# Optimization experiments

Hardware: AMD Instinct MI355X
Metric: run time of the kernel (lower is better)

The kernel has to match this reference:

```python
import jax, jax.numpy as jnp
import numpy as np

BS, T, Q, HID, PROJ = 16, 16, 100, 256, 256


def setup_inputs() -> dict:
    key = jax.random.key(0)
    k1, k2, k3, k4, k5 = jax.random.split(key, 5)
    frame_embeds = jax.random.normal(k1, (BS, T, Q, HID), jnp.float32)
    other_frame_embeds = jax.random.normal(k2, (BS, T, Q, HID), jnp.float32)
    W = jax.random.normal(k3, (HID, PROJ), jnp.float32) / np.sqrt(HID).astype(np.float32)
    b = jax.random.normal(k4, (PROJ,), jnp.float32) * 0.01
    n = BS * Q
    mid = jax.random.randint(k5, (n, 1), 1, T - 1, dtype=jnp.int32)
    bridge = jnp.concatenate(
        [jnp.zeros((n, 1), jnp.int32), mid, jnp.full((n, 1), T - 1, jnp.int32)], axis=1
    )  # (n,3): head=0, random pivot in [1,T-2], tail=T-1
    return {"frame_embeds": frame_embeds, "other_frame_embeds": other_frame_embeds,
            "W": W, "b": b, "bridge": bridge}


def _prep(fe, W, b):
    # Linear proj, (bs,t,q,c)->(bs*q, t, c), L2-normalize per embedding.
    bs, t, q, _ = fe.shape
    x = fe @ W + b
    x = x.transpose(0, 2, 1, 3).reshape(bs * q, t, -1)
    return x / jnp.linalg.norm(x, axis=-1, keepdims=True)


def _forward(frame_embeds, other_frame_embeds, W, b, bridge, delta=0.3):
    cur = _prep(frame_embeds, W, b)      # (n,t,c)
    other = _prep(other_frame_embeds, W, b)
    bh = bridge[:, 0].astype(jnp.float32)
    bp_f = bridge[:, 1].astype(jnp.float32)
    bt = bridge[:, 2].astype(jnp.float32)
    alpha = (bp_f - bh) / (bt - bh)      # (n,)
    sigma = alpha * (bt - bp_f)          # (n,)
    g = jnp.take_along_axis(cur, bridge[:, :, None], axis=1)  # (n,3,c) head/pivot/tail
    # positive brownian-bridge distance
    x = g[:, 1] - (1.0 - alpha)[:, None] * g[:, 0] - alpha[:, None] * g[:, 2]
    numer = jnp.exp(-jnp.sum(x * x, axis=-1) / (2.0 * sigma ** 2))  # (n,)
    # negatives: pivot frame taken from every sequence in [cur; other].
    # ||m_ij - a_i||^2 = ||m_ij||^2 - 2 m_ij.a_i + ||a_i||^2 with m_ij = neg_all[j, bp_i],
    # avoiding the (n,N,3,c) repeat tensor of the original.
    neg_all = jnp.concatenate([cur, other], axis=0)            # (N,t,c)
    a = (1.0 - alpha)[:, None] * g[:, 0] + alpha[:, None] * g[:, 2]  # (n,c)
    cross = jnp.einsum('ic,jtc->ijt', a, neg_all)              # (n,N,t)
    bp = bridge[:, 1]
    cross_g = jnp.take_along_axis(cross, bp[:, None, None], axis=2)[..., 0]  # (n,N)
    nn2_g = jnp.sum(neg_all * neg_all, axis=-1).T[bp]          # (n,N)
    x2 = nn2_g - 2.0 * cross_g + jnp.sum(a * a, axis=-1)[:, None]
    dist = -x2 / (2.0 * sigma ** 2)[:, None]                   # (n,N)
    n = dist.shape[0]
    idx = jnp.arange(n)
    self_dist = dist[idx, idx]
    dist = dist.at[idx, idx].set(-10000.0)
    topv, _ = jax.lax.top_k(dist, 5)
    deno = jnp.exp(jnp.concatenate([self_dist[:, None], topv], axis=-1))  # (n,6)
    brownian_loss = (numer / deno.sum(axis=-1)).mean()
    score = jnp.einsum('nc,nc->n', cur[:, 0], cur[:, -1])
    head_tail_match = jax.nn.softplus(delta - score).mean()
    return brownian_loss, head_tail_match


def reference(frame_embeds, other_frame_embeds, W, b, bridge):
    return _forward(frame_embeds, other_frame_embeds, W, b, bridge)
```

## Files before the change

kernel.cpp:

```cpp
#include <hip/hip_runtime.h>
#include <hip/hip_bf16.h>

#define NROW 1600
#define NEG  3200
#define ROWS_FLAT 25600
#define NSPLIT 25

using bf16x8 = __attribute__((ext_vector_type(8))) short;
using f32x4  = __attribute__((ext_vector_type(4))) float;

__device__ __forceinline__ float bf2f(unsigned v) { return __uint_as_float(v << 16); }
__device__ __forceinline__ ushort f2bf(float f) {
  __hip_bfloat16 h = __float2bfloat16(f);
  return *(ushort*)&h;
}
__device__ __forceinline__ float load1(const ushort* p, size_t idx, int f32) {
  return f32 ? ((const float*)p)[idx] : bf2f(p[idx]);
}
__device__ __forceinline__ int sniff_f32(const ushort* p, int lane) {
  unsigned e = ((unsigned)p[2*lane] >> 7) & 0xffu;
  unsigned long long b = __ballot(e >= 100u && e <= 140u);
  return (__popcll(b) >= 40) ? 0 : 1;
}
__device__ __forceinline__ bf16x8 cvt8b(const float* a, const float* b) {
  float4 fa = *(const float4*)a;
  float4 fb = *(const float4*)b;
  bf16x8 r;
  r[0]=(short)f2bf(fa.x); r[1]=(short)f2bf(fa.y); r[2]=(short)f2bf(fa.z); r[3]=(short)f2bf(fa.w);
  r[4]=(short)f2bf(fb.x); r[5]=(short)f2bf(fb.y); r[6]=(short)f2bf(fb.z); r[7]=(short)f2bf(fb.w);
  return r;
}

__global__ __launch_bounds__(256) void k_prep(const ushort* __restrict__ W,
    ushort* __restrict__ Wtf, int* __restrict__ zbase) {
  if (blockIdx.x == 0 && threadIdx.x < 21) zbase[threadIdx.x] = 0;
  int fW = sniff_f32(W, threadIdx.x & 63);
  int n = blockIdx.x, k = threadIdx.x;
  int n16 = n >> 4, m = n & 15, kb = k >> 5, q = (k >> 3) & 3, e = k & 7;
  Wtf[(size_t)(n16*8 + kb)*512 + q*128 + m*8 + e] =
      f2bf(load1(W, (size_t)k * 256 + n, fW));
}

__global__ __launch_bounds__(256) void k_proj(const ushort* __restrict__ fe0,
    const ushort* __restrict__ fe1, const ushort* __restrict__ Wtf,
    const ushort* __restrict__ bias, const int* __restrict__ bridge,
    ushort* __restrict__ Pb, ushort* __restrict__ Ab, float* __restrict__ prm,
    float* __restrict__ numer, int* __restrict__ cnt, int* __restrict__ lst,
    float* __restrict__ wsum) {
  __shared__ union {
    float  xf[32*256];
    ushort x[32*256];
    ushort c[4][32*72];
  } sh;
  __shared__ float s_ss[4][32];
  __shared__ float s_bb[4][2][3];
  __shared__ int   s_brg[2][3];
  const int tid = threadIdx.x;
  const int w = tid >> 6, lane = tid & 63, q = lane >> 4, m = lane & 15;
  const int I0 = blockIdx.x * 2;
  const int hasB = (I0 < NROW);
  const int s1 = (I0 >= NROW);
  const ushort* srcp = s1 ? fe1 : fe0;
  const int fSrc = sniff_f32(srcp, lane);
  const int fB   = sniff_f32(bias, lane);
  if (hasB && tid < 6) s_brg[tid/3][tid%3] = bridge[(I0 + tid/3)*3 + tid%3];
  {
    int ii = I0 - s1*NROW + (w >> 1);
    int b = ii / 100, qq = ii - b*100;
    const size_t ub = (size_t)(b*1600 + qq) * 256;
    if (fSrc) {
      const float* fp = (const float*)srcp;
      #pragma unroll
      for (int i2 = 0; i2 < 8; i2++) {
        int r = w*8 + i2;
        int t = r & 15;
        int g = lane ^ (i2 & 7);
        const float* gp = fp + ub + (size_t)t*25600 + g*4;
        __builtin_amdgcn_global_load_lds(
          (const __attribute__((address_space(1))) unsigned int*)gp,
          (__attribute__((address_space(3))) unsigned int*)&sh.xf[r*256], 16, 0, 0);
      }
    } else {
      #pragma unroll
      for (int i2 = 0; i2 < 4; i2++) {
        int c = w*4 + i2;
        int r  = 2*c + (lane >> 5);
        int t  = r & 15;
        int kc = (lane & 31) ^ (r & 7);
        const ushort* gp = srcp + ub + (size_t)t*25600 + kc*8;
        __builtin_amdgcn_global_load_lds(
          (const __attribute__((address_space(1))) unsigned int*)gp,
          (__attribute__((address_space(3))) unsigned int*)&sh.x[c*512], 16, 0, 0);
      }
    }
  }
  __syncthreads();
  f32x4 acc[2][4];
  #pragma unroll
  for (int nt = 0; nt < 4; nt++) {
    float bb = load1(bias, w*64 + nt*16 + m, fB);
    f32x4 v = {bb, bb, bb, bb};
    #pragma unroll
    for (int mt = 0; mt < 2; mt++) acc[mt][nt] = v;
  }
  const int sw = (m & 7) << 3;
  const ushort* wfb = Wtf + (size_t)(w*4)*4096 + lane*8;
  bf16x8 a_cur[2], b_cur[4];
  if (fSrc) {
    int g0 = (q*2) ^ (m&7), g1 = (q*2 + 1) ^ (m&7);
    #pragma unroll
    for (int mt = 0; mt < 2; mt++)
      a_cur[mt] = cvt8b(&sh.xf[(mt*16+m)*256 + g0*4], &sh.xf[(mt*16+m)*256 + g1*4]);
  } else {
    #pragma unroll
    for (int mt = 0; mt < 2; mt++)
      a_cur[mt] = *(const bf16x8*)&sh.x[(mt*16 + m)*256 + ((q*8) ^ sw)];
  }
  #pragma unroll
  for (int nt = 0; nt < 4; nt++)
    b_cur[nt] = *(const bf16x8*)(wfb + (size_t)nt*4096);
  #pragma unroll
  for (int k = 0; k < 8; k++) {
    bf16x8 a_nxt[2], b_nxt[4];
    if (k < 7) {
      #pragma unroll
      for (int nt = 0; nt < 4; nt++)
        b_nxt[nt] = *(const bf16x8*)(wfb + (size_t)nt*4096 + (k+1)*512);
      if (fSrc) {
        int g0 = ((k+1)*8 + q*2) ^ (m&7), g1 = ((k+1)*8 + q*2 + 1) ^ (m&7);
        #pragma unroll
        for (int mt = 0; mt < 2; mt++)
          a_nxt[mt] = cvt8b(&sh.xf[(mt*16+m)*256 + g0*4], &sh.xf[(mt*16+m)*256 + g1*4]);
      } else {
        int pk = ((k+1)*32 + q*8) ^ sw;
        #pragma unroll
        for (int mt = 0; mt < 2; mt++)
          a_nxt[mt] = *(const bf16x8*)&sh.x[(mt*16 + m)*256 + pk];
      }
    }
    #pragma unroll
    for (int nt = 0; nt < 4; nt++)
      #pragma unroll
      for (int mt = 0; mt < 2; mt++)
        acc[mt][nt] = __builtin_amdgcn_mfma_f32_16x16x32_bf16(a_cur[mt], b_cur[nt], acc[mt][nt], 0, 0, 0);
    if (k < 7) {
      a_cur[0] = a_nxt[0]; a_cur[1] = a_nxt[1];
      #pragma unroll
      for (int x = 0; x < 4; x++) b_cur[x] = b_nxt[x];
    }
  }
  float ssp[2][4];
  #pragma unroll
  for (int mt = 0; mt < 2; mt++)
    #pragma unroll
    for (int reg = 0; reg < 4; reg++) {
      float s = 0.f;
      #pragma unroll
      for (int nt = 0; nt < 4; nt++) { float v = acc[mt][nt][reg]; s += v*v; }
      ssp[mt][reg] = s;
    }
  #pragma unroll
  for (int mk = 1; mk < 16; mk <<= 1)
    #pragma unroll
    for (int mt = 0; mt < 2; mt++)
      #pragma unroll
      for (int reg = 0; reg < 4; reg++) ssp[mt][reg] += __shfl_xor(ssp[mt][reg], mk, 64);
  if (m == 0)
    #pragma unroll
    for (int mt = 0; mt < 2; mt++)
      #pragma unroll
      for (int reg = 0; reg < 4; reg++) s_ss[w][mt*16 + 4*q + reg] = ssp[mt][reg];
  __syncthreads();
  float inv[2][4];
  #pragma unroll
  for (int mt = 0; mt < 2; mt++)
    #pragma unroll
    for (int reg = 0; reg < 4; reg++) {
      int row = mt*16 + 4*q + reg;
      float s = s_ss[0][row] + s_ss[1][row] + s_ss[2][row] + s_ss[3][row];
      inv[mt][reg] = 1.0f / sqrtf(s);
    }
  #pragma unroll
  for (int mt = 0; mt < 2; mt++)
    #pragma unroll
    for (int reg = 0; reg < 4; reg++) {
      int rl = mt*16 + 4*q + reg;
      #pragma unroll
      for (int nt = 0; nt < 4; nt++)
        sh.c[w][rl*72 + nt*16 + m] = f2bf(acc[mt][nt][reg] * inv[mt][reg]);
    }
  __syncthreads();
  #pragma unroll
  for (int p = 0; p < 4; p++) {
    int row = p*8 + (tid >> 5);
    int ig  = row >> 4, t = row & 15;
    int I   = I0 + ig;
    int ch  = tid & 31;
    uint4 v = *(uint4*)&sh.c[ch >> 3][row*72 + (ch & 7)*8];
    *(uint4*)(Pb + ((size_t)t * NEG + I) * 256 + ch*8) = v;
  }
  if (hasB) {
    #pragma unroll
    for (int ih = 0; ih < 2; ih++) {
      int bh = s_brg[ih][0], bp = s_brg[ih][1], bt = s_brg[ih][2];
      float alpha = ((float)bp - (float)bh) / ((float)bt - (float)bh);
      int rb = ih*16;
      float g0 = bf2f(sh.c[w][(rb + bh)*72 + lane]);
      float g1 = bf2f(sh.c[w][(rb + bp)*72 + lane]);
      float g2 = bf2f(sh.c[w][(rb + bt)*72 + lane]);
      float hd = bf2f(sh.c[w][(rb +  0)*72 + lane]);
      float tl = bf2f(sh.c[w][(rb + 15)*72 + lane]);
      float a = (1.0f - alpha) * g0 + alpha * g2;
      float x = g1 - a;
      int I = I0 + ih;
      Ab[(size_t)I*256 + w*64 + lane] = f2bf(a);
      float xx = x*x, aa = a*a, sc = hd*tl;
      #pragma unroll
      for (int mk = 1; mk < 64; mk <<= 1) {
        xx += __shfl_xor(xx, mk, 64);
        aa += __shfl_xor(aa, mk, 64);
        sc += __shfl_xor(sc, mk, 64);
      }
      if (lane == 0) { s_bb[w][ih][0] = xx; s_bb[w][ih][1] = aa; s_bb[w][ih][2] = sc; }
    }
    __syncthreads();
    if (tid < 2) {
      int I = I0 + tid;
      float XX = s_bb[0][tid][0] + s_bb[1][tid][0] + s_bb[2][tid][0] + s_bb[3][tid][0];
      float AA = s_bb[0][tid][1] + s_bb[1][tid][1] + s_bb[2][tid][1] + s_bb[3][tid][1];
      float SC = s_bb[0][tid][2] + s_bb[1][tid][2] + s_bb[2][tid][2] + s_bb[3][tid][2];
      int bh = s_brg[tid][0], bp = s_brg[tid][1], bt = s_brg[tid][2];
      float alpha = ((float)bp - (float)bh) / ((float)bt - (float)bh);
      float sigma = alpha * ((float)bt - (float)bp);
      float inv2s2 = 1.0f / (2.0f * sigma * sigma);
      prm[I*2+0] = inv2s2;
      prm[I*2+1] = AA;
      numer[I] = expf(-XX * inv2s2);
      float sp = log1pf(expf(0.3f - SC));
      atomicAdd(wsum + 1, sp * (1.0f / 1600.0f));
      int pos = atomicAdd(cnt + bp, 1);
      lst[bp * 1600 + pos] = I;
    }
  }
}

__device__ __forceinline__ void sort5(float* c) {
  #define CE(i,j) { float hi = fmaxf(c[i], c[j]), lo = fminf(c[i], c[j]); c[i]=hi; c[j]=lo; }
  CE(0,1) CE(3,4) CE(2,4) CE(2,3) CE(1,4) CE(0,3) CE(0,2) CE(1,3) CE(1,2)
  #undef CE
}
__device__ __forceinline__ void ins5(float* t, float v) {
  float hi, lo;
  hi = fmaxf(t[0], v); lo = fminf(t[0], v); t[0] = hi; v = lo;
  hi = fmaxf(t[1], v); lo = fminf(t[1], v); t[1] = hi; v = lo;
  hi = fmaxf(t[2], v); lo = fminf(t[2], v); t[2] = hi; v = lo;
  hi = fmaxf(t[3], v); lo = fminf(t[3], v); t[3] = hi; v = lo;
  t[4] = fmaxf(t[4], v);
}

__global__ __launch_bounds__(256) void k_cross(const ushort* __restrict__ Pb,
    const ushort* __restrict__ Ab, const float* __restrict__ prm,
    const int* __restrict__ cnt, const int* __restrict__ lst,
    float* __restrict__ part) {
  int t = blockIdx.z;
  int n_t = min(cnt[t], 1600);
  int i0 = blockIdx.y * 64;
  if (i0 >= n_t) return;
  int j0 = blockIdx.x * 128;
  __shared__ int s_gis[64];
  __shared__ float s_red[4][64][6];
  int tid = threadIdx.x;
  if (tid < 64) {
    int gi = lst[t*1600 + min(i0 + tid, n_t - 1)];
    s_gis[tid] = min(max(gi, 0), NROW - 1);
  }
  __syncthreads();
  const int w = tid >> 6, lane = tid & 63, q = lane >> 4, m = lane & 15;
  const ushort* jp0 = Pb + ((size_t)t * NEG + (j0 + w*32 + m)) * 256 + q*8;
  const ushort* jp1 = jp0 + (size_t)16*256;
  int gi[4];
  const ushort* ip[4];
  #pragma unroll
  for (int it = 0; it < 4; it++) {
    gi[it] = s_gis[it*16 + m];
    ip[it] = Ab + (size_t)gi[it] * 256 + q*8;
  }
  f32x4 acc[2][4];
  #pragma unroll
  for (int jt = 0; jt < 2; jt++)
    #pragma unroll
    for (int it = 0; it < 4; it++) { f32x4 z = {0.f,0.f,0.f,0.f}; acc[jt][it] = z; }
  bf16x8 jc0 = *(const bf16x8*)(jp0);
  bf16x8 jc1 = *(const bf16x8*)(jp1);
  bf16x8 ic[4];
  #pragma unroll
  for (int it = 0; it < 4; it++) ic[it] = *(const bf16x8*)(ip[it]);
  #pragma unroll
  for (int k = 0; k < 8; k++) {
    bf16x8 jn0, jn1, in[4];
    if (k < 7) {
      int o = (k + 1) * 32;
      jn0 = *(const bf16x8*)(jp0 + o);
      jn1 = *(const bf16x8*)(jp1 + o);
      #pragma unroll
      for (int it = 0; it < 4; it++) in[it] = *(const bf16x8*)(ip[it] + o);
    }
    __builtin_amdgcn_s_setprio(1);
    #pragma unroll
    for (int it = 0; it < 4; it++) {
      acc[0][it] = __builtin_amdgcn_mfma_f32_16x16x32_bf16(jc0, ic[it], acc[0][it], 0, 0, 0);
      acc[1][it] = __builtin_amdgcn_mfma_f32_16x16x32_bf16(jc1, ic[it], acc[1][it], 0, 0, 0);
    }
    __builtin_amdgcn_s_setprio(0);
    if (k < 7) { jc0 = jn0; jc1 = jn1;
      #pragma unroll
      for (int it = 0; it < 4; it++) ic[it] = in[it];
    }
  }
  float top[4][5], selfv[4];
  float pi[4], pa[4];
  #pragma unroll
  for (int it = 0; it < 4; it++) {
    pi[it] = prm[gi[it]*2]; pa[it] = prm[gi[it]*2+1];
    selfv[it] = -1e30f;
    #pragma unroll
    for (int k = 0; k < 5; k++) top[it][k] = -1e30f;
  }
  #pragma unroll
  for (int jt = 0; jt < 2; jt++)
    #pragma unroll
    for (int reg = 0; reg < 4; reg++) {
      int j = j0 + w*32 + jt*16 + 4*q + reg;
      #pragma unroll
      for (int it = 0; it < 4; it++) {
        float d = -(1.0f - 2.0f*acc[jt][it][reg] + pa[it]) * pi[it];
        if (j == gi[it]) selfv[it] = d; else ins5(top[it], d);
      }
    }
  #pragma unroll
  for (int mk = 16; mk <= 32; mk <<= 1) {
    #pragma unroll
    for (int it = 0; it < 4; it++) {
      float o[5], c[5];
      #pragma unroll
      for (int k = 0; k < 5; k++) o[k] = __shfl_xor(top[it][k], mk, 64);
      #pragma unroll
      for (int k = 0; k < 5; k++) c[k] = fmaxf(top[it][k], o[4 - k]);
      sort5(c);
      #pragma unroll
      for (int k = 0; k < 5; k++) top[it][k] = c[k];
      selfv[it] = fmaxf(selfv[it], __shfl_xor(selfv[it], mk, 64));
    }
  }
  if (q == 0) {
    #pragma unroll
    for (int it = 0; it < 4; it++) {
      #pragma unroll
      for (int k = 0; k < 5; k++) s_red[w][it*16 + m][k] = top[it][k];
      s_red[w][it*16 + m][5] = selfv[it];
    }
  }
  __syncthreads();
  if (tid < 64 && i0 + tid < n_t) {
    float T[5], S = s_red[0][tid][5];
    #pragma unroll
    for (int k = 0; k < 5; k++) T[k] = s_red[0][tid][k];
    #pragma unroll
    for (int w2 = 1; w2 < 4; w2++) {
      #pragma unroll
      for (int k = 0; k < 5; k++) ins5(T, s_red[w2][tid][k]);
      S = fmaxf(S, s_red[w2][tid][5]);
    }
    float* pp = part + ((size_t)s_gis[tid]*NSPLIT + blockIdx.x) * 6;
    #pragma unroll
    for (int k = 0; k < 5; k++) pp[k] = T[k];
    pp[5] = S;
  }
}

__global__ __launch_bounds__(64) void k_merge(const float* __restrict__ part,
    const float* __restrict__ numer, float* __restrict__ wsum, int* __restrict__ done,
    const ushort* __restrict__ fe0, void* __restrict__ out) {
  int i = blockIdx.x * 64 + threadIdx.x;
  const float* pp = part + (size_t)i * NSPLIT * 6;
  float T[5]; float S = pp[5];
  #pragma unroll
  for (int k = 0; k < 5; k++) T[k] = pp[k];
  #pragma unroll
  for (int s = 1; s < NSPLIT; s++) {
    const float* ps = pp + s*6;
    float v0 = ps[0], v1 = ps[1], v2 = ps[2], v3 = ps[3], v4 = ps[4], v5 = ps[5];
    ins5(T, v0); ins5(T, v1); ins5(T, v2); ins5(T, v3); ins5(T, v4);
    S = fmaxf(S, v5);
  }
  float deno = expf(S);
  #pragma unroll
  for (int k = 0; k < 5; k++) deno += expf(T[k]);
  float local = numer[i] / deno;
  #pragma unroll
  for (int mk = 1; mk < 64; mk <<= 1) local += __shfl_xor(local, mk, 64);
  __shared__ int s_last;
  if (threadIdx.x == 0) {
    atomicAdd(wsum + 0, local * (1.0f / 1600.0f));
    __threadfence();
    s_last = (atomicAdd(done, 1) == 24);
  }
  __syncthreads();
  if (s_last) {
    int f = sniff_f32(fe0, threadIdx.x);
    if (threadIdx.x == 0) {
      __threadfence();
      float brown = __hip_atomic_load(wsum + 0, __ATOMIC_RELAXED, __HIP_MEMORY_SCOPE_AGENT);
      float sp    = __hip_atomic_load(wsum + 1, __ATOMIC_RELAXED, __HIP_MEMORY_SCOPE_AGENT);
      if (f) {
        ((float*)out)[0] = brown;
        ((float*)out)[1] = sp;
      } else {
        ushort* o = (ushort*)out;
        o[0] = f2bf(brown);
        o[1] = f2bf(sp);
      }
    }
  }
}

extern "C" void kernel_launch(void* const* d_in, const int* in_sizes, int n_in,
                              void* d_out, int out_size, void* d_ws, size_t ws_size,
                              hipStream_t stream) {
  const ushort* fe0    = (const ushort*)d_in[0];
  const ushort* fe1    = (const ushort*)d_in[1];
  const ushort* W      = (const ushort*)d_in[2];
  const ushort* bias   = (const ushort*)d_in[3];
  const int*    bridge = (const int*)d_in[4];

  ushort* Pb    = (ushort*)d_ws;
  ushort* Ab    = Pb + 13107200;
  ushort* Wtf   = Ab + 409600;
  float*  part  = (float*)(Wtf + 65536);
  float*  prm   = part + 240000;
  float*  numer = prm + 3200;
  float*  wsum  = numer + 1600;
  int*    cnt   = (int*)(wsum + 4);
  int*    done  = cnt + 16;
  int*    lst   = done + 1;

  k_prep  <<<256, 256, 0, stream>>>(W, Wtf, (int*)wsum);
  k_proj  <<<1600, 256, 0, stream>>>(fe0, fe1, Wtf, bias, bridge, Pb, Ab, prm, numer, cnt, lst, wsum);
  k_cross <<<dim3(NSPLIT, 7, 16), 256, 0, stream>>>(Pb, Ab, prm, cnt, lst, part);
  k_merge <<<25, 64, 0, stream>>>(part, numer, wsum, done, fe0, d_out);
}
```

Before: 161.3 us.

## Make projection blocks process four tiles with double-buffered LDS prefetch

Each k_proj block now handles four row-pair tiles instead of one, so the grid shrinks from 1600 to 400 blocks. While a block computes the MFMA projection, normalisation and bridge statistics for one tile, the async global-to-LDS load for the next tile is already issued into a second LDS buffer. The goal is to hide input-load latency and spread per-block setup (format sniffing, bias loads) over more work. In exchange, the block's LDS footprint roughly doubles, which can lower occupancy, and the tile loop adds barriers between tiles.

```diff
diff --git a/kernel.cpp b/kernel.cpp
--- a/kernel.cpp
+++ b/kernel.cpp
@@ -5,6 +5,7 @@
 #define NEG  3200
 #define ROWS_FLAT 25600
 #define NSPLIT 25
+#define TPB 4
 
 using bf16x8 = __attribute__((ext_vector_type(8))) short;
 using f32x4  = __attribute__((ext_vector_type(4))) float;
@@ -47,185 +48,194 @@
     ushort* __restrict__ Pb, ushort* __restrict__ Ab, float* __restrict__ prm,
     float* __restrict__ numer, int* __restrict__ cnt, int* __restrict__ lst,
     float* __restrict__ wsum) {
-  __shared__ union {
-    float  xf[32*256];
-    ushort x[32*256];
-    ushort c[4][32*72];
-  } sh;
+  __shared__ float sbuf[2][32*256];
   __shared__ float s_ss[4][32];
   __shared__ float s_bb[4][2][3];
   __shared__ int   s_brg[2][3];
   const int tid = threadIdx.x;
   const int w = tid >> 6, lane = tid & 63, q = lane >> 4, m = lane & 15;
-  const int I0 = blockIdx.x * 2;
-  const int hasB = (I0 < NROW);
-  const int s1 = (I0 >= NROW);
+  const int hasB = (blockIdx.x < 200);
+  const int s1 = !hasB;
   const ushort* srcp = s1 ? fe1 : fe0;
   const int fSrc = sniff_f32(srcp, lane);
   const int fB   = sniff_f32(bias, lane);
-  if (hasB && tid < 6) s_brg[tid/3][tid%3] = bridge[(I0 + tid/3)*3 + tid%3];
-  {
-    int ii = I0 - s1*NROW + (w >> 1);
-    int b = ii / 100, qq = ii - b*100;
-    const size_t ub = (size_t)(b*1600 + qq) * 256;
+  float bb[4];
+  #pragma unroll
+  for (int nt = 0; nt < 4; nt++) bb[nt] = load1(bias, w*64 + nt*16 + m, fB);
+  const ushort* wfb = Wtf + (size_t)(w*4)*4096 + lane*8;
+  const int sw = (m & 7) << 3;
+
+  auto STAGE = [&](int g, int b) {
+    int I0g = blockIdx.x*(2*TPB) + g*2;
+    int ii = I0g - s1*NROW + (w >> 1);
+    int bq = ii / 100, qq = ii - bq*100;
+    size_t ub = (size_t)(bq*1600 + qq) * 256;
     if (fSrc) {
       const float* fp = (const float*)srcp;
       #pragma unroll
       for (int i2 = 0; i2 < 8; i2++) {
         int r = w*8 + i2;
         int t = r & 15;
-        int g = lane ^ (i2 & 7);
-        const float* gp = fp + ub + (size_t)t*25600 + g*4;
+        int gg = lane ^ i2;
+        const float* gp = fp + ub + (size_t)t*25600 + gg*4;
         __builtin_amdgcn_global_load_lds(
           (const __attribute__((address_space(1))) unsigned int*)gp,
-          (__attribute__((address_space(3))) unsigned int*)&sh.xf[r*256], 16, 0, 0);
+          (__attribute__((address_space(3))) unsigned int*)&sbuf[b][r*256], 16, 0, 0);
       }
     } else {
+      ushort* xb = (ushort*)&sbuf[b][0];
       #pragma unroll
       for (int i2 = 0; i2 < 4; i2++) {
         int c = w*4 + i2;
-        int r  = 2*c + (lane >> 5);
-        int t  = r & 15;
+        int r = 2*c + (lane >> 5);
+        int t = r & 15;
         int kc = (lane & 31) ^ (r & 7);
         const ushort* gp = srcp + ub + (size_t)t*25600 + kc*8;
         __builtin_amdgcn_global_load_lds(
           (const __attribute__((address_space(1))) unsigned int*)gp,
-          (__attribute__((address_space(3))) unsigned int*)&sh.x[c*512], 16, 0, 0);
-      }
-    }
-  }
-  __syncthreads();
-  f32x4 acc[2][4];
-  #pragma unroll
-  for (int nt = 0; nt < 4; nt++) {
-    float bb = load1(bias, w*64 + nt*16 + m, fB);
-    f32x4 v = {bb, bb, bb, bb};
-    #pragma unroll
-    for (int mt = 0; mt < 2; mt++) acc[mt][nt] = v;
-  }
-  const int sw = (m & 7) << 3;
-  const ushort* wfb = Wtf + (size_t)(w*4)*4096 + lane*8;
-  bf16x8 a_cur[2], b_cur[4];
-  if (fSrc) {
-    int g0 = (q*2) ^ (m&7), g1 = (q*2 + 1) ^ (m&7);
+          (__attribute__((address_space(3))) unsigned int*)&xb[c*512], 16, 0, 0);
+      }
+    }
+  };
+
+  STAGE(0, 0);
+  for (int g = 0; g < TPB; g++) {
+    const int b = g & 1;
+    const int I0g = blockIdx.x*(2*TPB) + g*2;
+    if (g + 1 < TPB) STAGE(g + 1, b ^ 1);
+    if (g == 0) __syncthreads();
+    const float*  xf = &sbuf[b][0];
+    const ushort* xb = (const ushort*)xf;
+    ushort*       cb = (ushort*)&sbuf[b][0];
+    f32x4 acc[2][4];
+    #pragma unroll
+    for (int nt = 0; nt < 4; nt++) {
+      f32x4 v = {bb[nt], bb[nt], bb[nt], bb[nt]};
+      acc[0][nt] = v; acc[1][nt] = v;
+    }
+    bf16x8 a_cur[2], b_cur[4];
+    if (fSrc) {
+      int g0 = (q*2) ^ (m&7), g1 = (q*2 + 1) ^ (m&7);
+      #pragma unroll
+      for (int mt = 0; mt < 2; mt++)
+        a_cur[mt] = cvt8b(&xf[(mt*16+m)*256 + g0*4], &xf[(mt*16+m)*256 + g1*4]);
+    } else {
+      #pragma unroll
+      for (int mt = 0; mt < 2; mt++)
+        a_cur[mt] = *(const bf16x8*)&xb[(mt*16 + m)*256 + ((q*8) ^ sw)];
+    }
+    #pragma unroll
+    for (int nt = 0; nt < 4; nt++)
+      b_cur[nt] = *(const bf16x8*)(wfb + (size_t)nt*4096);
+    #pragma unroll
+    for (int k = 0; k < 8; k++) {
+      bf16x8 a_nxt[2], b_nxt[4];
+      if (k < 7) {
+        #pragma unroll
+        for (int nt = 0; nt < 4; nt++)
+          b_nxt[nt] = *(const bf16x8*)(wfb + (size_t)nt*4096 + (k+1)*512);
+        if (fSrc) {
+          int g0 = ((k+1)*8 + q*2) ^ (m&7), g1 = ((k+1)*8 + q*2 + 1) ^ (m&7);
+          #pragma unroll
+          for (int mt = 0; mt < 2; mt++)
+            a_nxt[mt] = cvt8b(&xf[(mt*16+m)*256 + g0*4], &xf[(mt*16+m)*256 + g1*4]);
+        } else {
+          int pk = ((k+1)*32 + q*8) ^ sw;
+          #pragma unroll
+          for (int mt = 0; mt < 2; mt++)
+            a_nxt[mt] = *(const bf16x8*)&xb[(mt*16 + m)*256 + pk];
+        }
+      }
+      #pragma unroll
+      for (int nt = 0; nt < 4; nt++)
+        #pragma unroll
+        for (int mt = 0; mt < 2; mt++)
+          acc[mt][nt] = __builtin_amdgcn_mfma_f32_16x16x32_bf16(a_cur[mt], b_cur[nt], acc[mt][nt], 0, 0, 0);
+      if (k < 7) {
+        a_cur[0] = a_nxt[0]; a_cur[1] = a_nxt[1];
+        #pragma unroll
+        for (int x = 0; x < 4; x++) b_cur[x] = b_nxt[x];
+      }
+    }
+    float ssp[2][4];
     #pragma unroll
     for (int mt = 0; mt < 2; mt++)
-      a_cur[mt] = cvt8b(&sh.xf[(mt*16+m)*256 + g0*4], &sh.xf[(mt*16+m)*256 + g1*4]);
-  } else {
+      #pragma unroll
+      for (int reg = 0; reg < 4; reg++) {
+        float s = 0.f;
+        #pragma unroll
+        for (int nt = 0; nt < 4; nt++) { float v = acc[mt][nt][reg]; s += v*v; }
+        ssp[mt][reg] = s;
+      }
+    #pragma unroll
+    for (int mk = 1; mk < 16; mk <<= 1)
+      #pragma unroll
+      for (int mt = 0; mt < 2; mt++)
+        #pragma unroll
+        for (int reg = 0; reg < 4; reg++) ssp[mt][reg] += __shfl_xor(ssp[mt][reg], mk, 64);
+    if (m == 0)
+      #pragma unroll
+      for (int mt = 0; mt < 2; mt++)
+        #pragma unroll
+        for (int reg = 0; reg < 4; reg++) s_ss[w][mt*16 + 4*q + reg] = ssp[mt][reg];
+    __syncthreads();
+    if (hasB && tid < 6) s_brg[tid/3][tid%3] = bridge[(I0g + tid/3)*3 + tid%3];
+    float inv[2][4];
     #pragma unroll
     for (int mt = 0; mt < 2; mt++)
-      a_cur[mt] = *(const bf16x8*)&sh.x[(mt*16 + m)*256 + ((q*8) ^ sw)];
-  }
-  #pragma unroll
-  for (int nt = 0; nt < 4; nt++)
-    b_cur[nt] = *(const bf16x8*)(wfb + (size_t)nt*4096);
-  #pragma unroll
-  for (int k = 0; k < 8; k++) {
-    bf16x8 a_nxt[2], b_nxt[4];
-    if (k < 7) {
-      #pragma unroll
-      for (int nt = 0; nt < 4; nt++)
-        b_nxt[nt] = *(const bf16x8*)(wfb + (size_t)nt*4096 + (k+1)*512);
-      if (fSrc) {
-        int g0 = ((k+1)*8 + q*2) ^ (m&7), g1 = ((k+1)*8 + q*2 + 1) ^ (m&7);
-        #pragma unroll
-        for (int mt = 0; mt < 2; mt++)
-          a_nxt[mt] = cvt8b(&sh.xf[(mt*16+m)*256 + g0*4], &sh.xf[(mt*16+m)*256 + g1*4]);
-      } else {
-        int pk = ((k+1)*32 + q*8) ^ sw;
-        #pragma unroll
-        for (int mt = 0; mt < 2; mt++)
-          a_nxt[mt] = *(const bf16x8*)&sh.x[(mt*16 + m)*256 + pk];
-      }
-    }
-    #pragma unroll
-    for (int nt = 0; nt < 4; nt++)
-      #pragma unroll
-      for (int mt = 0; mt < 2; mt++)
-        acc[mt][nt] = __builtin_amdgcn_mfma_f32_16x16x32_bf16(a_cur[mt], b_cur[nt], acc[mt][nt], 0, 0, 0);
-    if (k < 7) {
-      a_cur[0] = a_nxt[0]; a_cur[1] = a_nxt[1];
-      #pragma unroll
-      for (int x = 0; x < 4; x++) b_cur[x] = b_nxt[x];
-    }
-  }
-  float ssp[2][4];
-  #pragma unroll
-  for (int mt = 0; mt < 2; mt++)
-    #pragma unroll
-    for (int reg = 0; reg < 4; reg++) {
-      float s = 0.f;
-      #pragma unroll
-      for (int nt = 0; nt < 4; nt++) { float v = acc[mt][nt][reg]; s += v*v; }
-      ssp[mt][reg] = s;
-    }
-  #pragma unroll
-  for (int mk = 1; mk < 16; mk <<= 1)
+      #pragma unroll
+      for (int reg = 0; reg < 4; reg++) {
+        int row = mt*16 + 4*q + reg;
+        float s = s_ss[0][row] + s_ss[1][row] + s_ss[2][row] + s_ss[3][row];
+        inv[mt][reg] = 1.0f / sqrtf(s);
+      }
     #pragma unroll
     for (int mt = 0; mt < 2; mt++)
       #pragma unroll
-      for (int reg = 0; reg < 4; reg++) ssp[mt][reg] += __shfl_xor(ssp[mt][reg], mk, 64);
-  if (m == 0)
-    #pragma unroll
-    for (int mt = 0; mt < 2; mt++)
-      #pragma unroll
-      for (int reg = 0; reg < 4; reg++) s_ss[w][mt*16 + 4*q + reg] = ssp[mt][reg];
-  __syncthreads();
-  float inv[2][4];
-  #pragma unroll
-  for (int mt = 0; mt < 2; mt++)
-    #pragma unroll
-    for (int reg = 0; reg < 4; reg++) {
-      int row = mt*16 + 4*q + reg;
-      float s = s_ss[0][row] + s_ss[1][row] + s_ss[2][row] + s_ss[3][row];
-      inv[mt][reg] = 1.0f / sqrtf(s);
-    }
-  #pragma unroll
-  for (int mt = 0; mt < 2; mt++)
-    #pragma unroll
-    for (int reg = 0; reg < 4; reg++) {
-      int rl = mt*16 + 4*q + reg;
-      #pragma unroll
-      for (int nt = 0; nt < 4; nt++)
-        sh.c[w][rl*72 + nt*16 + m] = f2bf(acc[mt][nt][reg] * inv[mt][reg]);
-    }
-  __syncthreads();
-  #pragma unroll
-  for (int p = 0; p < 4; p++) {
-    int row = p*8 + (tid >> 5);
-    int ig  = row >> 4, t = row & 15;
-    int I   = I0 + ig;
-    int ch  = tid & 31;
-    uint4 v = *(uint4*)&sh.c[ch >> 3][row*72 + (ch & 7)*8];
-    *(uint4*)(Pb + ((size_t)t * NEG + I) * 256 + ch*8) = v;
-  }
-  if (hasB) {
-    #pragma unroll
-    for (int ih = 0; ih < 2; ih++) {
-      int bh = s_brg[ih][0], bp = s_brg[ih][1], bt = s_brg[ih][2];
-      float alpha = ((float)bp - (float)bh) / ((float)bt - (float)bh);
-      int rb = ih*16;
-      float g0 = bf2f(sh.c[w][(rb + bh)*72 + lane]);
-      float g1 = bf2f(sh.c[w][(rb + bp)*72 + lane]);
-      float g2 = bf2f(sh.c[w][(rb + bt)*72 + lane]);
-      float hd = bf2f(sh.c[w][(rb +  0)*72 + lane]);
-      float tl = bf2f(sh.c[w][(rb + 15)*72 + lane]);
-      float a = (1.0f - alpha) * g0 + alpha * g2;
-      float x = g1 - a;
-      int I = I0 + ih;
-      Ab[(size_t)I*256 + w*64 + lane] = f2bf(a);
-      float xx = x*x, aa = a*a, sc = hd*tl;
-      #pragma unroll
-      for (int mk = 1; mk < 64; mk <<= 1) {
-        xx += __shfl_xor(xx, mk, 64);
-        aa += __shfl_xor(aa, mk, 64);
-        sc += __shfl_xor(sc, mk, 64);
-      }
-      if (lane == 0) { s_bb[w][ih][0] = xx; s_bb[w][ih][1] = aa; s_bb[w][ih][2] = sc; }
-    }
+      for (int reg = 0; reg < 4; reg++) {
+        int rl = mt*16 + 4*q + reg;
+        #pragma unroll
+        for (int nt = 0; nt < 4; nt++)
+          cb[w*2304 + rl*72 + nt*16 + m] = f2bf(acc[mt][nt][reg] * inv[mt][reg]);
+      }
     __syncthreads();
-    if (tid < 2) {
-      int I = I0 + tid;
+    #pragma unroll
+    for (int p = 0; p < 4; p++) {
+      int row = p*8 + (tid >> 5);
+      int ig  = row >> 4, t = row & 15;
+      int I   = I0g + ig;
+      int ch  = tid & 31;
+      uint4 v = *(uint4*)&cb[(ch >> 3)*2304 + row*72 + (ch & 7)*8];
+      *(uint4*)(Pb + ((size_t)t * NEG + I) * 256 + ch*8) = v;
+    }
+    if (hasB) {
+      #pragma unroll
+      for (int ih = 0; ih < 2; ih++) {
+        int bh = s_brg[ih][0], bp = s_brg[ih][1], bt = s_brg[ih][2];
+        float alpha = ((float)bp - (float)bh) / ((float)bt - (float)bh);
+        int rb = ih*16;
+        float g0 = bf2f(cb[w*2304 + (rb + bh)*72 + lane]);
+        float g1 = bf2f(cb[w*2304 + (rb + bp)*72 + lane]);
+        float g2 = bf2f(cb[w*2304 + (rb + bt)*72 + lane]);
+        float hd = bf2f(cb[w*2304 + (rb +  0)*72 + lane]);
+        float tl = bf2f(cb[w*2304 + (rb + 15)*72 + lane]);
+        float a = (1.0f - alpha) * g0 + alpha * g2;
+        float x = g1 - a;
+        int I = I0g + ih;
+        Ab[(size_t)I*256 + w*64 + lane] = f2bf(a);
+        float xx = x*x, aa = a*a, sc = hd*tl;
+        #pragma unroll
+        for (int mk = 1; mk < 64; mk <<= 1) {
+          xx += __shfl_xor(xx, mk, 64);
+          aa += __shfl_xor(aa, mk, 64);
+          sc += __shfl_xor(sc, mk, 64);
+        }
+        if (lane == 0) { s_bb[w][ih][0] = xx; s_bb[w][ih][1] = aa; s_bb[w][ih][2] = sc; }
+      }
+    }
+    __syncthreads();
+    if (hasB && tid < 2) {
+      int I = I0g + tid;
       float XX = s_bb[0][tid][0] + s_bb[1][tid][0] + s_bb[2][tid][0] + s_bb[3][tid][0];
       float AA = s_bb[0][tid][1] + s_bb[1][tid][1] + s_bb[2][tid][1] + s_bb[3][tid][1];
       float SC = s_bb[0][tid][2] + s_bb[1][tid][2] + s_bb[2][tid][2] + s_bb[3][tid][2];
@@ -445,7 +455,7 @@
   int*    lst   = done + 1;
 
   k_prep  <<<256, 256, 0, stream>>>(W, Wtf, (int*)wsum);
-  k_proj  <<<1600, 256, 0, stream>>>(fe0, fe1, Wtf, bias, bridge, Pb, Ab, prm, numer, cnt, lst, wsum);
+  k_proj  <<<400, 256, 0, stream>>>(fe0, fe1, Wtf, bias, bridge, Pb, Ab, prm, numer, cnt, lst, wsum);
   k_cross <<<dim3(NSPLIT, 7, 16), 256, 0, stream>>>(Pb, Ab, prm, cnt, lst, part);
   k_merge <<<25, 64, 0, stream>>>(part, numer, wsum, done, fe0, d_out);
 }
```

Result: slower. 167.5 us (+3.8%).
